# Performance work log

Hardware: AMD Instinct MI355X
Metric: run time of the kernel (lower is better)

The kernel has to match this reference:

```python
import jax, jax.numpy as jnp
import numpy as np

I_DIM = 512   # encoder feature size fed to CfC
UNITS = 1024  # AutoNCP total units (hidden_dim)
OUT = 128     # motor neurons (output_dim)
N = [538, 358, 128]                      # inter, command, motor layer sizes
IN_TOT = [I_DIM + N[0], N[0] + N[1], N[1] + N[2]]  # concat(input, h) width per layer
B, T = 512, 128


def setup_inputs() -> dict:
    key = jax.random.key(0)
    ks = jax.random.split(key, 40)
    d = {}
    d["x"] = jax.random.normal(ks[0], (B, T, I_DIM), jnp.float32)
    d["h0"] = jnp.zeros((B, UNITS), jnp.float32)
    ki = 1
    for l in range(3):
        it, n = IN_TOT[l], N[l]
        sp = (jax.random.uniform(ks[ki], (n, it - n)) < 0.5).astype(jnp.float32); ki += 1
        d[f"mask{l}"] = jnp.concatenate([sp, jnp.ones((n, n), jnp.float32)], axis=1)
        for name in ("Wff1", "Wff2", "Wta", "Wtb"):
            d[f"{name}_{l}"] = jax.random.normal(ks[ki], (n, it), jnp.float32) * float(1.0 / np.sqrt(it)); ki += 1
        for name in ("bff1", "bff2", "bta", "btb"):
            d[f"{name}_{l}"] = jnp.zeros((n,), jnp.float32)
    d["Wfc"] = jax.random.normal(ks[ki], (OUT, OUT), jnp.float32) * float(1.0 / np.sqrt(OUT))
    d["bfc"] = jnp.zeros((OUT,), jnp.float32)
    return d


def _cell(xin, h, p):
    # CfCCell, mode='default', no backbone, ts = 1.0
    W1, b1, W2, b2, Wa, ba, Wb, bb = p
    xc = jnp.concatenate([xin, h], axis=-1)           # (B, in+n)
    ff1 = jnp.tanh(xc @ W1.T + b1)
    ff2 = jnp.tanh(xc @ W2.T + b2)
    t_interp = jax.nn.sigmoid((xc @ Wa.T + ba) + (xc @ Wb.T + bb))
    return ff1 * (1.0 - t_interp) + t_interp * ff2


def reference(x, h0, mask0, Wff1_0, Wff2_0, Wta_0, Wtb_0, bff1_0, bff2_0, bta_0, btb_0,
              mask1, Wff1_1, Wff2_1, Wta_1, Wtb_1, bff1_1, bff2_1, bta_1, btb_1,
              mask2, Wff1_2, Wff2_2, Wta_2, Wtb_2, bff1_2, bff2_2, bta_2, btb_2,
              Wfc, bfc):
    params = (
        (Wff1_0 * mask0, bff1_0, Wff2_0 * mask0, bff2_0, Wta_0, bta_0, Wtb_0, btb_0),
        (Wff1_1 * mask1, bff1_1, Wff2_1 * mask1, bff2_1, Wta_1, bta_1, Wtb_1, btb_1),
        (Wff1_2 * mask2, bff1_2, Wff2_2 * mask2, bff2_2, Wta_2, bta_2, Wtb_2, btb_2),
    )
    hs0 = tuple(jnp.split(h0, [N[0], N[0] + N[1]], axis=1))

    def step(hs, x_t):
        inp = x_t
        new = []
        for l in range(3):
            inp = _cell(inp, hs[l], params[l])
            new.append(inp)
        return tuple(new), inp  # last layer (motor) is the cell output

    carry, outs = jax.lax.scan(step, hs0, jnp.swapaxes(x, 0, 1))
    outputs = jnp.swapaxes(outs, 0, 1)        # (B, T, OUT)
    hn = jnp.concatenate(carry, axis=1)       # (B, UNITS)
    predictions = outputs @ Wfc.T + bfc       # final nn.Linear
    return predictions, hn
```

## Files before the change

kernel.cpp:

```cpp
#include <hip/hip_runtime.h>
#include <stdint.h>

typedef __attribute__((ext_vector_type(8))) short short8;
typedef __attribute__((ext_vector_type(4))) float float4v;
typedef __attribute__((ext_vector_type(4))) unsigned short ushort4v;

constexpr int T = 128;
constexpr int NB = 512;
constexpr int NCH = 16;
constexpr int CBLK = 12;
constexpr int HS = 1056;

__device__ __forceinline__ float bf2f(ushort u) {
  union { float f; uint32_t i; } v; v.i = ((uint32_t)u) << 16; return v.f;
}
__device__ __forceinline__ ushort f2bf(float f) {
  union { float f; uint32_t i; } v; v.f = f;
  uint32_t i = v.i;
  uint32_t r = i + 0x7FFFu + ((i >> 16) & 1u);
  return (ushort)(r >> 16);
}

__device__ __forceinline__ unsigned long long coh_load8(const float* p) {
  return __hip_atomic_load(
      reinterpret_cast<unsigned long long*>(const_cast<float*>(p)),
      __ATOMIC_RELAXED, __HIP_MEMORY_SCOPE_SYSTEM);
}
__device__ __forceinline__ void coh_store8(float* p, float a, float b) {
  union { unsigned long long u; float f[2]; } v; v.f[0] = a; v.f[1] = b;
  __hip_atomic_store(reinterpret_cast<unsigned long long*>(p), v.u,
                     __ATOMIC_RELAXED, __HIP_MEMORY_SCOPE_SYSTEM);
}

__global__ __launch_bounds__(256) void pack_w(const float* __restrict__ W,
                                              const float* __restrict__ mask,
                                              ushort* __restrict__ out, int loOff,
                                              int NN, int IT, int NT, int KB,
                                              int POLD, int OLDLEN, int SOFF,
                                              int NEWLEN) {
  int idx = blockIdx.x * 256 + threadIdx.x;
  int total = KB * NT * 512;
  if (idx >= total) return;
  int jj   = idx & 7;
  int lane = (idx >> 3) & 63;
  int nt   = (idx >> 9) % NT;
  int kb   = (idx >> 9) / NT;
  int n = nt * 16 + (lane & 15);
  int p = kb * 32 + (lane >> 4) * 8 + jj;
  int src = -1;
  if (p < POLD) {
    if (p < OLDLEN) src = SOFF + p;
  } else {
    int q = p - POLD;
    if (q < NEWLEN) src = q;
  }
  float v = 0.f;
  if (n < NN && src >= 0) {
    v = W[(size_t)n * IT + src];
    if (mask) v *= mask[(size_t)n * IT + src];
  }
  ushort hi = f2bf(v);
  out[idx] = hi;
  out[loOff + idx] = f2bf(v - bf2f(hi));
}

template <int NTW, bool COH, int KB0, int KB1, int KOFF>
__device__ __forceinline__ void cell_range(
    ushort* __restrict__ Ah, ushort* __restrict__ Al,
    const float* __restrict__ aRow,
    const ushort* __restrict__ wfq, int nt0, int NT, int loOff,
    float4v (&acc)[2][NTW]) {
  constexpr int PD = 4;
  constexpr int LEN = KB1 - KB0;
  const int tid  = threadIdx.x;
  const int lane = tid & 63, quad = lane >> 4, l16 = lane & 15;
  const int sm = tid >> 3;
  const int sk = (tid & 7) * 4;

  short8 cbh[PD][NTW], cbl[PD][NTW];
  float4v av[PD];

  auto loadB = [&](int kb, short8* bh, short8* bl) {
#pragma unroll
    for (int w = 0; w < NTW; w++) {
      const size_t fo = ((size_t)(kb * NT + nt0 + w) * 64 + lane) * 8;
      bh[w] = *(const short8*)(wfq + fo);
      bl[w] = *(const short8*)(wfq + loOff + fo);
    }
  };
  auto loadA = [&](int kb) -> float4v {
    const float* p = aRow + (kb - KOFF) * 32 + sk;
    float4v r;
    if (COH) {
      union { unsigned long long u; float f[2]; } x0, x1;
      x0.u = coh_load8(p);
      x1.u = coh_load8(p + 2);
      r[0] = x0.f[0]; r[1] = x0.f[1]; r[2] = x1.f[0]; r[3] = x1.f[1];
    } else {
      r = *(const float4v*)p;
    }
    return r;
  };

#pragma unroll
  for (int i = 0; i < PD; i++) { av[i] = loadA(KB0 + i); loadB(KB0 + i, cbh[i], cbl[i]); }

  for (int kb0 = KB0; kb0 < KB1; kb0 += PD) {
#pragma unroll
    for (int u = 0; u < PD; u++) {
      const int kb = kb0 + u;
      if ((LEN % PD) && kb >= KB1) continue;
      const int ab = (kb & 1) * 1280;

      ushort4v hi4, lo4;
#pragma unroll
      for (int e = 0; e < 4; e++) {
        float v = av[u][e];
        ushort hi = f2bf(v);
        hi4[e] = hi;
        lo4[e] = f2bf(v - bf2f(hi));
      }
      *(ushort4v*)(Ah + ab + sm * 40 + sk) = hi4;
      *(ushort4v*)(Al + ab + sm * 40 + sk) = lo4;
      asm volatile("s_waitcnt lgkmcnt(0)\n\ts_barrier" ::: "memory");

#pragma unroll
      for (int mt = 0; mt < 2; mt++) {
        short8 ah = *(const short8*)&Ah[ab + (mt * 16 + l16) * 40 + quad * 8];
        short8 al = *(const short8*)&Al[ab + (mt * 16 + l16) * 40 + quad * 8];
#pragma unroll
        for (int w = 0; w < NTW; w++) {
          acc[mt][w] = __builtin_amdgcn_mfma_f32_16x16x32_bf16(ah, cbh[u][w], acc[mt][w], 0, 0, 0);
          acc[mt][w] = __builtin_amdgcn_mfma_f32_16x16x32_bf16(al, cbh[u][w], acc[mt][w], 0, 0, 0);
          acc[mt][w] = __builtin_amdgcn_mfma_f32_16x16x32_bf16(ah, cbl[u][w], acc[mt][w], 0, 0, 0);
        }
      }
      if (kb + PD < KB1) { av[u] = loadA(kb + PD); loadB(kb + PD, cbh[u], cbl[u]); }
    }
  }
}

template <int NTW>
__device__ __forceinline__ void cell_epilogue(
    float* __restrict__ Acc, float4v (&acc)[2][NTW],
    const float* const* __restrict__ bias4,
    int NN, int NNPAD, float* __restrict__ hout, float* __restrict__ out2,
    int b0, int n0) {
  const int tid = threadIdx.x;
  const int wave = tid >> 6, lane = tid & 63, quad = lane >> 4, l16 = lane & 15;
#pragma unroll
  for (int mt = 0; mt < 2; mt++)
#pragma unroll
    for (int w = 0; w < NTW; w++)
#pragma unroll
      for (int r = 0; r < 4; r++)
        Acc[(wave * 32 + mt * 16 + quad * 4 + r) * 50 + w * 16 + l16] = acc[mt][w][r];
  __syncthreads();
  constexpr int CW = 16 * NTW;
  for (int i4 = tid; i4 < 32 * (CW / 4); i4 += 256) {
    const int r = i4 / (CW / 4);
    const int c4 = (i4 % (CW / 4)) * 4;
    const int j0 = n0 + c4;
    if (j0 >= NNPAD) continue;
    float hv[4];
#pragma unroll
    for (int e = 0; e < 4; e++) {
      const int c = c4 + e, j = j0 + e;
      float h = 0.f;
      if (j < NN) {
        float v1 = Acc[(0 * 32 + r) * 50 + c] + bias4[0][j];
        float v2 = Acc[(1 * 32 + r) * 50 + c] + bias4[1][j];
        float va = Acc[(2 * 32 + r) * 50 + c] + bias4[2][j];
        float vb = Acc[(3 * 32 + r) * 50 + c] + bias4[3][j];
        float ff1 = tanhf(v1);
        float ff2 = tanhf(v2);
        float s = 1.f / (1.f + expf(-(va + vb)));
        h = ff1 * (1.f - s) + s * ff2;
      }
      hv[e] = h;
    }
    float* hp = hout + (size_t)(b0 + r) * HS + j0;
    coh_store8(hp, hv[0], hv[1]);
    coh_store8(hp + 2, hv[2], hv[3]);
    if (out2) {
      float4v o; o[0] = hv[0]; o[1] = hv[1]; o[2] = hv[2]; o[3] = hv[3];
      *(float4v*)(out2 + (size_t)(b0 + r) * 16384 + j0) = o;
    }
  }
}

struct PParams {
  const float* x;
  float* h0; float* h1;
  const ushort* wf0[4]; const ushort* wf1[4]; const ushort* wf2[4];
  int loOff0, loOff1, loOff2;
  const float* bias0[4]; const float* bias1[4]; const float* bias2[4];
  float* pred;
  int* bar;
};

__device__ __forceinline__ void bar_arrive(int* slot) {
  asm volatile("s_waitcnt vmcnt(0)" ::: "memory");
  __syncthreads();
  if (threadIdx.x == 0)
    __hip_atomic_fetch_add(slot, 1, __ATOMIC_RELAXED, __HIP_MEMORY_SCOPE_SYSTEM);
}
__device__ __forceinline__ void bar_wait(int* slot, int target) {
  if (threadIdx.x == 0) {
    while (__hip_atomic_load(slot, __ATOMIC_RELAXED, __HIP_MEMORY_SCOPE_SYSTEM) < target)
      __builtin_amdgcn_s_sleep(1);
  }
  __syncthreads();
}

__global__ __launch_bounds__(256, 1) void cfc_persistent(PParams p) {
  __shared__ ushort Ah[2 * 32 * 40];
  __shared__ ushort Al[2 * 32 * 40];
  __shared__ float  Acc[4 * 32 * 50];
  const int blk = blockIdx.x;
  const int c = blk / CBLK, ntp = blk % CBLK;
  const int b0 = c * 32;
  int* cbar = p.bar + c * (T * 3);
  const int wave = threadIdx.x >> 6;
  const int sm = threadIdx.x >> 3;
  const size_t rowoff = (size_t)(b0 + sm);

  for (int t = 0; t < T; t++) {
    float* hr = (t & 1) ? p.h1 : p.h0;
    float* hw = (t & 1) ? p.h0 : p.h1;
    const float* xRow  = p.x + rowoff * (T * 512) + (size_t)t * 512;
    const float* hrRow = hr + rowoff * HS;
    const float* hwRow = hw + rowoff * HS;

    float4v acc0[2][3];
#pragma unroll
    for (int i = 0; i < 2; i++)
#pragma unroll
      for (int w = 0; w < 3; w++) acc0[i][w] = float4v{0.f, 0.f, 0.f, 0.f};
    cell_range<3, false, 0, 16, 0 >(Ah, Al, xRow,  p.wf0[wave], ntp * 3, 36, p.loOff0, acc0);
    cell_range<3, true, 16, 33, 16>(Ah, Al, hrRow, p.wf0[wave], ntp * 3, 36, p.loOff0, acc0);
    cell_epilogue<3>(Acc, acc0, p.bias0, 538, 544, hw, nullptr, b0, ntp * 48);
    bar_arrive(cbar + t * 3);

    if (t && ntp >= 4) bar_wait(cbar + (t - 1) * 3 + 1, CBLK);
    float4v acc1[2][2];
#pragma unroll
    for (int i = 0; i < 2; i++)
#pragma unroll
      for (int w = 0; w < 2; w++) acc1[i][w] = float4v{0.f, 0.f, 0.f, 0.f};
    cell_range<2, true, 0, 12, 0 >(Ah, Al, hrRow + 544, p.wf1[wave], ntp * 2, 24, p.loOff1, acc1);
    bar_wait(cbar + t * 3, CBLK);
    cell_range<2, true, 12, 29, 12>(Ah, Al, hwRow, p.wf1[wave], ntp * 2, 24, p.loOff1, acc1);
    cell_epilogue<2>(Acc, acc1, p.bias1, 358, 384, hw + 544, nullptr, b0, ntp * 32);
    bar_arrive(cbar + t * 3 + 1);

    if (ntp < 4) {
      if (t) bar_wait(cbar + (t - 1) * 3 + 2, 4);
      float4v acc2[2][2];
#pragma unroll
      for (int i = 0; i < 2; i++)
#pragma unroll
        for (int w = 0; w < 2; w++) acc2[i][w] = float4v{0.f, 0.f, 0.f, 0.f};
      cell_range<2, true, 0, 4, 0>(Ah, Al, hrRow + 928, p.wf2[wave], ntp * 2, 8, p.loOff2, acc2);
      bar_wait(cbar + t * 3 + 1, CBLK);
      cell_range<2, true, 4, 16, 4>(Ah, Al, hwRow + 544, p.wf2[wave], ntp * 2, 8, p.loOff2, acc2);
      cell_epilogue<2>(Acc, acc2, p.bias2, 128, 128, hw + 928,
                       p.pred + (size_t)t * 128, b0, ntp * 32);
      bar_arrive(cbar + t * 3 + 2);
    }
  }
}

__global__ __launch_bounds__(256) void h_scatter(const float* __restrict__ src,
                                                 float* __restrict__ dst) {
  int idx = blockIdx.x * 256 + threadIdx.x;
  if (idx >= NB * HS) return;
  int b = idx / HS, u = idx % HS;
  int s = -1;
  if (u < 538) s = u;
  else if (u >= 544 && u < 902) s = 538 + (u - 544);
  else if (u >= 928) s = 896 + (u - 928);
  dst[idx] = (s >= 0) ? src[(size_t)b * 1024 + s] : 0.f;
}
__global__ __launch_bounds__(256) void h_gather(const float* __restrict__ src,
                                                float* __restrict__ dst) {
  int idx = blockIdx.x * 256 + threadIdx.x;
  if (idx >= NB * 1024) return;
  int b = idx / 1024, u = idx % 1024;
  int pu = (u < 538) ? u : (u < 896 ? (u - 538) + 544 : (u - 896) + 928);
  dst[idx] = src[(size_t)b * HS + pu];
}

__global__ __launch_bounds__(256)
void final_linear(float* __restrict__ io, const ushort* __restrict__ wfc_frag,
                  int loOff, const float* __restrict__ bfc) {
  __shared__ ushort Ah[64][136];
  __shared__ ushort Al[64][136];
  const int tid = threadIdx.x;
  const int wave = tid >> 6, lane = tid & 63, quad = lane >> 4, l16 = lane & 15;
  const size_t r0 = (size_t)blockIdx.x * 64;
  {
    const int row = tid >> 2;
    const int cb  = (tid & 3) * 32;
    const float* src = io + (r0 + row) * 128 + cb;
#pragma unroll
    for (int e = 0; e < 32; e++) {
      float v = src[e];
      ushort hi = f2bf(v);
      Ah[row][cb + e] = hi;
      Al[row][cb + e] = f2bf(v - bf2f(hi));
    }
  }
  __syncthreads();
  float4v acc[8];
#pragma unroll
  for (int i = 0; i < 8; i++) acc[i] = float4v{0.f, 0.f, 0.f, 0.f};
#pragma unroll
  for (int kb = 0; kb < 4; kb++) {
    short8 ah = *(const short8*)&Ah[wave * 16 + l16][kb * 32 + quad * 8];
    short8 al = *(const short8*)&Al[wave * 16 + l16][kb * 32 + quad * 8];
#pragma unroll
    for (int nt = 0; nt < 8; nt++) {
      const size_t fo = ((size_t)(kb * 8 + nt) * 64 + lane) * 8;
      short8 bh = *(const short8*)(wfc_frag + fo);
      short8 bl = *(const short8*)(wfc_frag + loOff + fo);
      acc[nt] = __builtin_amdgcn_mfma_f32_16x16x32_bf16(ah, bh, acc[nt], 0, 0, 0);
      acc[nt] = __builtin_amdgcn_mfma_f32_16x16x32_bf16(al, bh, acc[nt], 0, 0, 0);
      acc[nt] = __builtin_amdgcn_mfma_f32_16x16x32_bf16(ah, bl, acc[nt], 0, 0, 0);
    }
  }
  __syncthreads();
#pragma unroll
  for (int nt = 0; nt < 8; nt++) {
    int col = nt * 16 + l16;
    float bb = bfc[col];
#pragma unroll
    for (int r = 0; r < 4; r++) {
      int row = wave * 16 + quad * 4 + r;
      io[(r0 + row) * 128 + col] = acc[nt][r] + bb;
    }
  }
}

extern "C" void kernel_launch(void* const* d_in, const int* in_sizes, int n_in,
                              void* d_out, int out_size, void* d_ws, size_t ws_size,
                              hipStream_t stream) {
  const int maskIdx[3] = {2, 11, 20};
  const int wIdx[3]    = {3, 12, 21};
  const float* Wfc = (const float*)d_in[29];
  const float* bfc = (const float*)d_in[30];

  const int KBs[3]  = {33, 29, 16};
  const int NTs[3]  = {36, 24, 8};
  const int NNs[3]  = {538, 358, 128};
  const int ITs[3]  = {1050, 896, 486};
  const int POLDs[3]   = {0, 384, 128};
  const int OLDLENs[3] = {0, 358, 128};
  const int SOFFs[3]   = {0, 538, 358};
  const int NEWLENs[3] = {1050, 538, 358};

  ushort* ws = (ushort*)d_ws;
  size_t off = 0;
  ushort* wf[3][4];
  int loOff[3];
  for (int l = 0; l < 3; l++) {
    loOff[l] = KBs[l] * NTs[l] * 512;
    for (int q = 0; q < 4; q++) {
      wf[l][q] = ws + off;
      off += (size_t)2 * loOff[l];
    }
  }
  int wfcLo = 4 * 8 * 512;
  ushort* wfc_f = ws + off; off += (size_t)2 * wfcLo;
  float* hb0 = (float*)(ws + off); off += (size_t)NB * HS * 2;
  float* hb1 = (float*)(ws + off); off += (size_t)NB * HS * 2;
  int* bar = (int*)(ws + off); off += (size_t)NCH * T * 3 * 2;

  float* pred = (float*)d_out;
  float* hn   = (float*)d_out + (size_t)NB * T * 128;

  for (int l = 0; l < 3; l++) {
    int blocks = (loOff[l] + 255) / 256;
    for (int q = 0; q < 4; q++) {
      const float* m = (q < 2) ? (const float*)d_in[maskIdx[l]] : nullptr;
      pack_w<<<blocks, 256, 0, stream>>>((const float*)d_in[wIdx[l] + q], m, wf[l][q],
                                         loOff[l], NNs[l], ITs[l], NTs[l], KBs[l],
                                         POLDs[l], OLDLENs[l], SOFFs[l], NEWLENs[l]);
    }
  }
  pack_w<<<(wfcLo + 255) / 256, 256, 0, stream>>>(Wfc, nullptr, wfc_f, wfcLo,
                                                  128, 128, 8, 4, 0, 0, 0, 128);

  hipMemsetAsync(bar, 0, NCH * T * 3 * sizeof(int), stream);
  h_scatter<<<(NB * HS + 255) / 256, 256, 0, stream>>>((const float*)d_in[1], hb0);

  PParams p;
  p.x = (const float*)d_in[0];
  p.h0 = hb0; p.h1 = hb1;
  for (int q = 0; q < 4; q++) {
    p.wf0[q] = wf[0][q]; p.wf1[q] = wf[1][q]; p.wf2[q] = wf[2][q];
    p.bias0[q] = (const float*)d_in[7 + q];
    p.bias1[q] = (const float*)d_in[16 + q];
    p.bias2[q] = (const float*)d_in[25 + q];
  }
  p.loOff0 = loOff[0]; p.loOff1 = loOff[1]; p.loOff2 = loOff[2];
  p.pred = pred;
  p.bar = bar;

  cfc_persistent<<<NCH * CBLK, 256, 0, stream>>>(p);

  final_linear<<<(NB * T) / 64, 256, 0, stream>>>(pred, wfc_f, wfcLo, bfc);
  h_gather<<<(NB * 1024 + 255) / 256, 256, 0, stream>>>(hb0, hn);
}
```

Measured before the change: 5.867 ms.

## Halve per-step barriers, narrow atomic scope to agent, remap blocks across XCDs

The K-loop now stages two k-blocks into four LDS slots per barrier instead of one, which cuts workgroup barriers in the recurrent GEMM roughly in half. An odd trailing block is handled after the loop, and a sync is added before the epilogue. Coherent loads, stores and the inter-block barrier atomics drop from system scope to agent scope, which should make them cheaper. Block IDs are also remapped so the 12 blocks of each batch chunk are spread by XCD-interleaved index. The agent-scope change assumes every participant sits on one device, and the remap changes which blocks share an L2.

```diff
diff --git a/kernel.cpp b/kernel.cpp
--- a/kernel.cpp
+++ b/kernel.cpp
@@ -24,12 +24,12 @@
 __device__ __forceinline__ unsigned long long coh_load8(const float* p) {
   return __hip_atomic_load(
       reinterpret_cast<unsigned long long*>(const_cast<float*>(p)),
-      __ATOMIC_RELAXED, __HIP_MEMORY_SCOPE_SYSTEM);
+      __ATOMIC_RELAXED, __HIP_MEMORY_SCOPE_AGENT);
 }
 __device__ __forceinline__ void coh_store8(float* p, float a, float b) {
   union { unsigned long long u; float f[2]; } v; v.f[0] = a; v.f[1] = b;
   __hip_atomic_store(reinterpret_cast<unsigned long long*>(p), v.u,
-                     __ATOMIC_RELAXED, __HIP_MEMORY_SCOPE_SYSTEM);
+                     __ATOMIC_RELAXED, __HIP_MEMORY_SCOPE_AGENT);
 }
 
 __global__ __launch_bounds__(256) void pack_w(const float* __restrict__ W,
@@ -66,12 +66,14 @@
 
 template <int NTW, bool COH, int KB0, int KB1, int KOFF>
 __device__ __forceinline__ void cell_range(
-    ushort* __restrict__ Ah, ushort* __restrict__ Al,
+    ushort* __restrict__ Ast,
     const float* __restrict__ aRow,
     const ushort* __restrict__ wfq, int nt0, int NT, int loOff,
     float4v (&acc)[2][NTW]) {
   constexpr int PD = 4;
   constexpr int LEN = KB1 - KB0;
+  constexpr int LEN2 = LEN & ~1;
+  static_assert(LEN2 % PD == 0, "even part of every segment must be x4");
   const int tid  = threadIdx.x;
   const int lane = tid & 63, quad = lane >> 4, l16 = lane & 15;
   const int sm = tid >> 3;
@@ -80,7 +82,7 @@
   short8 cbh[PD][NTW], cbl[PD][NTW];
   float4v av[PD];
 
-  auto loadB = [&](int kb, short8* bh, short8* bl) {
+  auto loadB = [&](int kb, short8 (&bh)[NTW], short8 (&bl)[NTW]) {
 #pragma unroll
     for (int w = 0; w < NTW; w++) {
       const size_t fo = ((size_t)(kb * NT + nt0 + w) * 64 + lane) * 8;
@@ -101,42 +103,53 @@
     }
     return r;
   };
+  auto stageSlot = [&](int u, float4v a) {
+    ushort4v hi4, lo4;
+#pragma unroll
+    for (int e = 0; e < 4; e++) {
+      float v = a[e];
+      ushort hi = f2bf(v);
+      hi4[e] = hi;
+      lo4[e] = f2bf(v - bf2f(hi));
+    }
+    *(ushort4v*)(Ast + u * 2560 + sm * 40 + sk) = hi4;
+    *(ushort4v*)(Ast + u * 2560 + 1280 + sm * 40 + sk) = lo4;
+  };
+  auto mfmaSlot = [&](int u, const short8 (&bh)[NTW], const short8 (&bl)[NTW]) {
+#pragma unroll
+    for (int mt = 0; mt < 2; mt++) {
+      short8 ah = *(const short8*)(Ast + u * 2560 + (mt * 16 + l16) * 40 + quad * 8);
+      short8 al = *(const short8*)(Ast + u * 2560 + 1280 + (mt * 16 + l16) * 40 + quad * 8);
+#pragma unroll
+      for (int w = 0; w < NTW; w++) {
+        acc[mt][w] = __builtin_amdgcn_mfma_f32_16x16x32_bf16(ah, bh[w], acc[mt][w], 0, 0, 0);
+        acc[mt][w] = __builtin_amdgcn_mfma_f32_16x16x32_bf16(al, bh[w], acc[mt][w], 0, 0, 0);
+        acc[mt][w] = __builtin_amdgcn_mfma_f32_16x16x32_bf16(ah, bl[w], acc[mt][w], 0, 0, 0);
+      }
+    }
+  };
 
 #pragma unroll
   for (int i = 0; i < PD; i++) { av[i] = loadA(KB0 + i); loadB(KB0 + i, cbh[i], cbl[i]); }
 
-  for (int kb0 = KB0; kb0 < KB1; kb0 += PD) {
-#pragma unroll
-    for (int u = 0; u < PD; u++) {
-      const int kb = kb0 + u;
-      if ((LEN % PD) && kb >= KB1) continue;
-      const int ab = (kb & 1) * 1280;
-
-      ushort4v hi4, lo4;
-#pragma unroll
-      for (int e = 0; e < 4; e++) {
-        float v = av[u][e];
-        ushort hi = f2bf(v);
-        hi4[e] = hi;
-        lo4[e] = f2bf(v - bf2f(hi));
-      }
-      *(ushort4v*)(Ah + ab + sm * 40 + sk) = hi4;
-      *(ushort4v*)(Al + ab + sm * 40 + sk) = lo4;
+  for (int kb0 = KB0; kb0 < KB0 + LEN2; kb0 += PD) {
+#pragma unroll
+    for (int up = 0; up < 2; up++) {
+      const int u0 = up * 2, u1 = up * 2 + 1;
+      const int kb = kb0 + up * 2;
+      stageSlot(u0, av[u0]);
+      stageSlot(u1, av[u1]);
       asm volatile("s_waitcnt lgkmcnt(0)\n\ts_barrier" ::: "memory");
-
-#pragma unroll
-      for (int mt = 0; mt < 2; mt++) {
-        short8 ah = *(const short8*)&Ah[ab + (mt * 16 + l16) * 40 + quad * 8];
-        short8 al = *(const short8*)&Al[ab + (mt * 16 + l16) * 40 + quad * 8];
-#pragma unroll
-        for (int w = 0; w < NTW; w++) {
-          acc[mt][w] = __builtin_amdgcn_mfma_f32_16x16x32_bf16(ah, cbh[u][w], acc[mt][w], 0, 0, 0);
-          acc[mt][w] = __builtin_amdgcn_mfma_f32_16x16x32_bf16(al, cbh[u][w], acc[mt][w], 0, 0, 0);
-          acc[mt][w] = __builtin_amdgcn_mfma_f32_16x16x32_bf16(ah, cbl[u][w], acc[mt][w], 0, 0, 0);
-        }
-      }
-      if (kb + PD < KB1) { av[u] = loadA(kb + PD); loadB(kb + PD, cbh[u], cbl[u]); }
-    }
+      mfmaSlot(u0, cbh[u0], cbl[u0]);
+      mfmaSlot(u1, cbh[u1], cbl[u1]);
+      if (kb + PD < KB1)     { av[u0] = loadA(kb + PD);     loadB(kb + PD,     cbh[u0], cbl[u0]); }
+      if (kb + 1 + PD < KB1) { av[u1] = loadA(kb + 1 + PD); loadB(kb + 1 + PD, cbh[u1], cbl[u1]); }
+    }
+  }
+  if (LEN & 1) {
+    stageSlot(0, av[0]);
+    asm volatile("s_waitcnt lgkmcnt(0)\n\ts_barrier" ::: "memory");
+    mfmaSlot(0, cbh[0], cbl[0]);
   }
 }
 
@@ -148,6 +161,7 @@
     int b0, int n0) {
   const int tid = threadIdx.x;
   const int wave = tid >> 6, lane = tid & 63, quad = lane >> 4, l16 = lane & 15;
+  __syncthreads();
 #pragma unroll
   for (int mt = 0; mt < 2; mt++)
 #pragma unroll
@@ -203,22 +217,23 @@
   asm volatile("s_waitcnt vmcnt(0)" ::: "memory");
   __syncthreads();
   if (threadIdx.x == 0)
-    __hip_atomic_fetch_add(slot, 1, __ATOMIC_RELAXED, __HIP_MEMORY_SCOPE_SYSTEM);
+    __hip_atomic_fetch_add(slot, 1, __ATOMIC_RELAXED, __HIP_MEMORY_SCOPE_AGENT);
 }
 __device__ __forceinline__ void bar_wait(int* slot, int target) {
   if (threadIdx.x == 0) {
-    while (__hip_atomic_load(slot, __ATOMIC_RELAXED, __HIP_MEMORY_SCOPE_SYSTEM) < target)
+    while (__hip_atomic_load(slot, __ATOMIC_RELAXED, __HIP_MEMORY_SCOPE_AGENT) < target)
       __builtin_amdgcn_s_sleep(1);
   }
   __syncthreads();
 }
 
 __global__ __launch_bounds__(256, 1) void cfc_persistent(PParams p) {
-  __shared__ ushort Ah[2 * 32 * 40];
-  __shared__ ushort Al[2 * 32 * 40];
+  __shared__ ushort Ast[4 * 2560];
   __shared__ float  Acc[4 * 32 * 50];
-  const int blk = blockIdx.x;
-  const int c = blk / CBLK, ntp = blk % CBLK;
+  const int phys = blockIdx.x;
+  const int s = (phys & 7) * 24 + (phys >> 3);
+  const int ntp = s >> 4;
+  const int c   = s & 15;
   const int b0 = c * 32;
   int* cbar = p.bar + c * (T * 3);
   const int wave = threadIdx.x >> 6;
@@ -237,8 +252,8 @@
     for (int i = 0; i < 2; i++)
 #pragma unroll
       for (int w = 0; w < 3; w++) acc0[i][w] = float4v{0.f, 0.f, 0.f, 0.f};
-    cell_range<3, false, 0, 16, 0 >(Ah, Al, xRow,  p.wf0[wave], ntp * 3, 36, p.loOff0, acc0);
-    cell_range<3, true, 16, 33, 16>(Ah, Al, hrRow, p.wf0[wave], ntp * 3, 36, p.loOff0, acc0);
+    cell_range<3, false, 0, 16, 0 >(Ast, xRow,  p.wf0[wave], ntp * 3, 36, p.loOff0, acc0);
+    cell_range<3, true, 16, 33, 16>(Ast, hrRow, p.wf0[wave], ntp * 3, 36, p.loOff0, acc0);
     cell_epilogue<3>(Acc, acc0, p.bias0, 538, 544, hw, nullptr, b0, ntp * 48);
     bar_arrive(cbar + t * 3);
 
@@ -248,9 +263,9 @@
     for (int i = 0; i < 2; i++)
 #pragma unroll
       for (int w = 0; w < 2; w++) acc1[i][w] = float4v{0.f, 0.f, 0.f, 0.f};
-    cell_range<2, true, 0, 12, 0 >(Ah, Al, hrRow + 544, p.wf1[wave], ntp * 2, 24, p.loOff1, acc1);
+    cell_range<2, true, 0, 12, 0 >(Ast, hrRow + 544, p.wf1[wave], ntp * 2, 24, p.loOff1, acc1);
     bar_wait(cbar + t * 3, CBLK);
-    cell_range<2, true, 12, 29, 12>(Ah, Al, hwRow, p.wf1[wave], ntp * 2, 24, p.loOff1, acc1);
+    cell_range<2, true, 12, 29, 12>(Ast, hwRow, p.wf1[wave], ntp * 2, 24, p.loOff1, acc1);
     cell_epilogue<2>(Acc, acc1, p.bias1, 358, 384, hw + 544, nullptr, b0, ntp * 32);
     bar_arrive(cbar + t * 3 + 1);
 
@@ -261,9 +276,9 @@
       for (int i = 0; i < 2; i++)
 #pragma unroll
         for (int w = 0; w < 2; w++) acc2[i][w] = float4v{0.f, 0.f, 0.f, 0.f};
-      cell_range<2, true, 0, 4, 0>(Ah, Al, hrRow + 928, p.wf2[wave], ntp * 2, 8, p.loOff2, acc2);
+      cell_range<2, true, 0, 4, 0>(Ast, hrRow + 928, p.wf2[wave], ntp * 2, 8, p.loOff2, acc2);
       bar_wait(cbar + t * 3 + 1, CBLK);
-      cell_range<2, true, 4, 16, 4>(Ah, Al, hwRow + 544, p.wf2[wave], ntp * 2, 8, p.loOff2, acc2);
+      cell_range<2, true, 4, 16, 4>(Ast, hwRow + 544, p.wf2[wave], ntp * 2, 8, p.loOff2, acc2);
       cell_epilogue<2>(Acc, acc2, p.bias2, 128, 128, hw + 928,
                        p.pred + (size_t)t * 128, b0, ntp * 32);
       bar_arrive(cbar + t * 3 + 2);
```

Result: faster. 5.749 ms (-2.0%).

## Store hidden state as split bf16 and stage whole A panels in LDS

Applied to the files above, without the earlier changes.

The hidden state is now kept in global memory as pre-split bf16 hi/lo pairs, written once in the epilogue, instead of fp32 values that every consumer had to split again. Each cell stage now copies the whole A operand (x or h segment) into a large LDS buffer up front. This replaces the per-k-block convert, LDS write and barrier loop with barrier-free double-buffered LDS reads inside the MFMA loop. Atomics and barriers are narrowed from system to agent scope, and blocks are remapped across chunks. In exchange there is more LDS, extra staging barriers, and an extra rounding step when h is stored as hi+lo.

```diff
diff --git a/kernel.cpp b/kernel.cpp
--- a/kernel.cpp
+++ b/kernel.cpp
@@ -21,15 +21,14 @@
   return (ushort)(r >> 16);
 }
 
-__device__ __forceinline__ unsigned long long coh_load8(const float* p) {
+__device__ __forceinline__ unsigned long long coh_load8u(const ushort* p) {
   return __hip_atomic_load(
-      reinterpret_cast<unsigned long long*>(const_cast<float*>(p)),
-      __ATOMIC_RELAXED, __HIP_MEMORY_SCOPE_SYSTEM);
-}
-__device__ __forceinline__ void coh_store8(float* p, float a, float b) {
-  union { unsigned long long u; float f[2]; } v; v.f[0] = a; v.f[1] = b;
-  __hip_atomic_store(reinterpret_cast<unsigned long long*>(p), v.u,
-                     __ATOMIC_RELAXED, __HIP_MEMORY_SCOPE_SYSTEM);
+      reinterpret_cast<unsigned long long*>(const_cast<ushort*>(p)),
+      __ATOMIC_RELAXED, __HIP_MEMORY_SCOPE_AGENT);
+}
+__device__ __forceinline__ void coh_store8u(ushort* p, unsigned long long v) {
+  __hip_atomic_store(reinterpret_cast<unsigned long long*>(p), v,
+                     __ATOMIC_RELAXED, __HIP_MEMORY_SCOPE_AGENT);
 }
 
 __global__ __launch_bounds__(256) void pack_w(const float* __restrict__ W,
@@ -64,78 +63,102 @@
   out[loOff + idx] = f2bf(v - bf2f(hi));
 }
 
-template <int NTW, bool COH, int KB0, int KB1, int KOFF>
-__device__ __forceinline__ void cell_range(
-    ushort* __restrict__ Ah, ushort* __restrict__ Al,
-    const float* __restrict__ aRow,
-    const ushort* __restrict__ wfq, int nt0, int NT, int loOff,
-    float4v (&acc)[2][NTW]) {
-  constexpr int PD = 4;
-  constexpr int LEN = KB1 - KB0;
-  const int tid  = threadIdx.x;
-  const int lane = tid & 63, quad = lane >> 4, l16 = lane & 15;
-  const int sm = tid >> 3;
-  const int sk = (tid & 7) * 4;
+template <int SEGC, int S>
+__device__ __forceinline__ void stage_h(ushort* __restrict__ Abuf,
+                                        const ushort* __restrict__ hiG,
+                                        const ushort* __restrict__ loG) {
+  constexpr int CH = SEGC / 32;
+  const int r  = threadIdx.x >> 3;
+  const int c0 = (threadIdx.x & 7) * (SEGC / 8);
+  const ushort* hg = hiG + (size_t)r * HS + c0;
+  const ushort* lg = loG + (size_t)r * HS + c0;
+  unsigned long long vh[CH], vl[CH];
+#pragma unroll
+  for (int i = 0; i < CH; i++) vh[i] = coh_load8u(hg + i * 4);
+#pragma unroll
+  for (int i = 0; i < CH; i++) vl[i] = coh_load8u(lg + i * 4);
+  ushort* hd = Abuf + r * S + c0;
+  ushort* ld = Abuf + 32 * S + r * S + c0;
+#pragma unroll
+  for (int i = 0; i < CH; i++) *(unsigned long long*)(hd + i * 4) = vh[i];
+#pragma unroll
+  for (int i = 0; i < CH; i++) *(unsigned long long*)(ld + i * 4) = vl[i];
+}
+
+template <int S>
+__device__ __forceinline__ void stage_x(ushort* __restrict__ Abuf,
+                                        const float* __restrict__ xG) {
+  const int r = threadIdx.x >> 3;
+  const int q = threadIdx.x & 7;
+  const float* src = xG + (size_t)r * (T * 512);
+  ushort* hd = Abuf + r * S;
+  ushort* ld = Abuf + 32 * S + r * S;
+#pragma unroll
+  for (int i = 0; i < 8; i++) {
+    const int c = q * 8 + i * 64;
+    float4v a = *(const float4v*)(src + c);
+    float4v b = *(const float4v*)(src + c + 4);
+    ushort4v ha, la, hb, lb;
+#pragma unroll
+    for (int e = 0; e < 4; e++) {
+      ushort h1 = f2bf(a[e]); ha[e] = h1; la[e] = f2bf(a[e] - bf2f(h1));
+      ushort h2 = f2bf(b[e]); hb[e] = h2; lb[e] = f2bf(b[e] - bf2f(h2));
+    }
+    *(ushort4v*)(hd + c) = ha; *(ushort4v*)(hd + c + 4) = hb;
+    *(ushort4v*)(ld + c) = la; *(ushort4v*)(ld + c + 4) = lb;
+  }
+}
+
+template <int NTW, int PD, int KB0, int KB1, int KOFF, int S>
+__device__ __forceinline__ void krange(const ushort* __restrict__ Abuf,
+                                       const ushort* __restrict__ wfq, int nt0,
+                                       int NT, int loOff, float4v (&acc)[2][NTW]) {
+  static_assert((PD & 1) == 0 && (KB0 & 1) == 0, "static parity needs even");
+  const int lane = threadIdx.x & 63, quad = lane >> 4, l16 = lane & 15;
+  const int ab = l16 * S + quad * 8 - KOFF * 32;
 
   short8 cbh[PD][NTW], cbl[PD][NTW];
-  float4v av[PD];
-
-  auto loadB = [&](int kb, short8* bh, short8* bl) {
+  short8 ah[2][2], al[2][2];
+
+  auto loadB = [&](int kb, int u) {
 #pragma unroll
     for (int w = 0; w < NTW; w++) {
       const size_t fo = ((size_t)(kb * NT + nt0 + w) * 64 + lane) * 8;
-      bh[w] = *(const short8*)(wfq + fo);
-      bl[w] = *(const short8*)(wfq + loOff + fo);
+      cbh[u][w] = *(const short8*)(wfq + fo);
+      cbl[u][w] = *(const short8*)(wfq + loOff + fo);
     }
   };
-  auto loadA = [&](int kb) -> float4v {
-    const float* p = aRow + (kb - KOFF) * 32 + sk;
-    float4v r;
-    if (COH) {
-      union { unsigned long long u; float f[2]; } x0, x1;
-      x0.u = coh_load8(p);
-      x1.u = coh_load8(p + 2);
-      r[0] = x0.f[0]; r[1] = x0.f[1]; r[2] = x1.f[0]; r[3] = x1.f[1];
-    } else {
-      r = *(const float4v*)p;
-    }
-    return r;
+  auto dsA = [&](int kb, int par) {
+    const int o = ab + kb * 32;
+    ah[par][0] = *(const short8*)(Abuf + o);
+    ah[par][1] = *(const short8*)(Abuf + o + 16 * S);
+    al[par][0] = *(const short8*)(Abuf + o + 32 * S);
+    al[par][1] = *(const short8*)(Abuf + o + 48 * S);
   };
 
 #pragma unroll
-  for (int i = 0; i < PD; i++) { av[i] = loadA(KB0 + i); loadB(KB0 + i, cbh[i], cbl[i]); }
+  for (int i = 0; i < PD; i++)
+    if (KB0 + i < KB1) loadB(KB0 + i, i);
+  dsA(KB0, 0);
 
   for (int kb0 = KB0; kb0 < KB1; kb0 += PD) {
 #pragma unroll
     for (int u = 0; u < PD; u++) {
       const int kb = kb0 + u;
-      if ((LEN % PD) && kb >= KB1) continue;
-      const int ab = (kb & 1) * 1280;
-
-      ushort4v hi4, lo4;
-#pragma unroll
-      for (int e = 0; e < 4; e++) {
-        float v = av[u][e];
-        ushort hi = f2bf(v);
-        hi4[e] = hi;
-        lo4[e] = f2bf(v - bf2f(hi));
+      if (kb < KB1) {
+        const int par = (KB0 + u) & 1;
+        if (kb + 1 < KB1) dsA(kb + 1, par ^ 1);
+#pragma unroll
+        for (int mt = 0; mt < 2; mt++) {
+#pragma unroll
+          for (int w = 0; w < NTW; w++) {
+            acc[mt][w] = __builtin_amdgcn_mfma_f32_16x16x32_bf16(ah[par][mt], cbh[u][w], acc[mt][w], 0, 0, 0);
+            acc[mt][w] = __builtin_amdgcn_mfma_f32_16x16x32_bf16(al[par][mt], cbh[u][w], acc[mt][w], 0, 0, 0);
+            acc[mt][w] = __builtin_amdgcn_mfma_f32_16x16x32_bf16(ah[par][mt], cbl[u][w], acc[mt][w], 0, 0, 0);
+          }
+        }
+        if (kb + PD < KB1) loadB(kb + PD, u);
       }
-      *(ushort4v*)(Ah + ab + sm * 40 + sk) = hi4;
-      *(ushort4v*)(Al + ab + sm * 40 + sk) = lo4;
-      asm volatile("s_waitcnt lgkmcnt(0)\n\ts_barrier" ::: "memory");
-
-#pragma unroll
-      for (int mt = 0; mt < 2; mt++) {
-        short8 ah = *(const short8*)&Ah[ab + (mt * 16 + l16) * 40 + quad * 8];
-        short8 al = *(const short8*)&Al[ab + (mt * 16 + l16) * 40 + quad * 8];
-#pragma unroll
-        for (int w = 0; w < NTW; w++) {
-          acc[mt][w] = __builtin_amdgcn_mfma_f32_16x16x32_bf16(ah, cbh[u][w], acc[mt][w], 0, 0, 0);
-          acc[mt][w] = __builtin_amdgcn_mfma_f32_16x16x32_bf16(al, cbh[u][w], acc[mt][w], 0, 0, 0);
-          acc[mt][w] = __builtin_amdgcn_mfma_f32_16x16x32_bf16(ah, cbl[u][w], acc[mt][w], 0, 0, 0);
-        }
-      }
-      if (kb + PD < KB1) { av[u] = loadA(kb + PD); loadB(kb + PD, cbh[u], cbl[u]); }
     }
   }
 }
@@ -144,10 +167,11 @@
 __device__ __forceinline__ void cell_epilogue(
     float* __restrict__ Acc, float4v (&acc)[2][NTW],
     const float* const* __restrict__ bias4,
-    int NN, int NNPAD, float* __restrict__ hout, float* __restrict__ out2,
-    int b0, int n0) {
+    int NN, int NNPAD, ushort* __restrict__ hiOut, ushort* __restrict__ loOut,
+    float* __restrict__ out2, int b0, int n0) {
   const int tid = threadIdx.x;
   const int wave = tid >> 6, lane = tid & 63, quad = lane >> 4, l16 = lane & 15;
+  __syncthreads();
 #pragma unroll
   for (int mt = 0; mt < 2; mt++)
 #pragma unroll
@@ -162,6 +186,7 @@
     const int c4 = (i4 % (CW / 4)) * 4;
     const int j0 = n0 + c4;
     if (j0 >= NNPAD) continue;
+    union { ushort u[4]; unsigned long long ll; } ph, pl;
     float hv[4];
 #pragma unroll
     for (int e = 0; e < 4; e++) {
@@ -178,10 +203,13 @@
         h = ff1 * (1.f - s) + s * ff2;
       }
       hv[e] = h;
-    }
-    float* hp = hout + (size_t)(b0 + r) * HS + j0;
-    coh_store8(hp, hv[0], hv[1]);
-    coh_store8(hp + 2, hv[2], hv[3]);
+      ushort hh = f2bf(h);
+      ph.u[e] = hh;
+      pl.u[e] = f2bf(h - bf2f(hh));
+    }
+    const size_t ro = (size_t)(b0 + r) * HS + j0;
+    coh_store8u(hiOut + ro, ph.ll);
+    coh_store8u(loOut + ro, pl.ll);
     if (out2) {
       float4v o; o[0] = hv[0]; o[1] = hv[1]; o[2] = hv[2]; o[3] = hv[3];
       *(float4v*)(out2 + (size_t)(b0 + r) * 16384 + j0) = o;
@@ -191,7 +219,7 @@
 
 struct PParams {
   const float* x;
-  float* h0; float* h1;
+  ushort* h0hi; ushort* h0lo; ushort* h1hi; ushort* h1lo;
   const ushort* wf0[4]; const ushort* wf1[4]; const ushort* wf2[4];
   int loOff0, loOff1, loOff2;
   const float* bias0[4]; const float* bias1[4]; const float* bias2[4];
@@ -203,68 +231,85 @@
   asm volatile("s_waitcnt vmcnt(0)" ::: "memory");
   __syncthreads();
   if (threadIdx.x == 0)
-    __hip_atomic_fetch_add(slot, 1, __ATOMIC_RELAXED, __HIP_MEMORY_SCOPE_SYSTEM);
+    __hip_atomic_fetch_add(slot, 1, __ATOMIC_RELAXED, __HIP_MEMORY_SCOPE_AGENT);
 }
 __device__ __forceinline__ void bar_wait(int* slot, int target) {
   if (threadIdx.x == 0) {
-    while (__hip_atomic_load(slot, __ATOMIC_RELAXED, __HIP_MEMORY_SCOPE_SYSTEM) < target)
+    while (__hip_atomic_load(slot, __ATOMIC_RELAXED, __HIP_MEMORY_SCOPE_AGENT) < target)
       __builtin_amdgcn_s_sleep(1);
   }
   __syncthreads();
 }
 
 __global__ __launch_bounds__(256, 1) void cfc_persistent(PParams p) {
-  __shared__ ushort Ah[2 * 32 * 40];
-  __shared__ ushort Al[2 * 32 * 40];
+  __shared__ ushort Abuf[2 * 32 * 552];
   __shared__ float  Acc[4 * 32 * 50];
-  const int blk = blockIdx.x;
-  const int c = blk / CBLK, ntp = blk % CBLK;
+  const int phys = blockIdx.x;
+  const int s = (phys & 7) * 24 + (phys >> 3);
+  const int ntp = s >> 4;
+  const int c   = s & 15;
   const int b0 = c * 32;
   int* cbar = p.bar + c * (T * 3);
   const int wave = threadIdx.x >> 6;
-  const int sm = threadIdx.x >> 3;
-  const size_t rowoff = (size_t)(b0 + sm);
+  const ushort* wq0 = p.wf0[wave];
+  const ushort* wq1 = p.wf1[wave];
+  const ushort* wq2 = p.wf2[wave];
+  const size_t bo = (size_t)b0 * HS;
 
   for (int t = 0; t < T; t++) {
-    float* hr = (t & 1) ? p.h1 : p.h0;
-    float* hw = (t & 1) ? p.h0 : p.h1;
-    const float* xRow  = p.x + rowoff * (T * 512) + (size_t)t * 512;
-    const float* hrRow = hr + rowoff * HS;
-    const float* hwRow = hw + rowoff * HS;
-
+    const bool odd = t & 1;
+    const ushort* rdHi = odd ? p.h1hi : p.h0hi;
+    const ushort* rdLo = odd ? p.h1lo : p.h0lo;
+    ushort* wrHi = odd ? p.h0hi : p.h1hi;
+    ushort* wrLo = odd ? p.h0lo : p.h1lo;
+
+    stage_x<520>(Abuf, p.x + (size_t)b0 * (T * 512) + (size_t)t * 512);
+    __syncthreads();
     float4v acc0[2][3];
 #pragma unroll
     for (int i = 0; i < 2; i++)
 #pragma unroll
       for (int w = 0; w < 3; w++) acc0[i][w] = float4v{0.f, 0.f, 0.f, 0.f};
-    cell_range<3, false, 0, 16, 0 >(Ah, Al, xRow,  p.wf0[wave], ntp * 3, 36, p.loOff0, acc0);
-    cell_range<3, true, 16, 33, 16>(Ah, Al, hrRow, p.wf0[wave], ntp * 3, 36, p.loOff0, acc0);
-    cell_epilogue<3>(Acc, acc0, p.bias0, 538, 544, hw, nullptr, b0, ntp * 48);
+    krange<3, 4, 0, 16, 0, 520>(Abuf, wq0, ntp * 3, 36, p.loOff0, acc0);
+    __syncthreads();
+    stage_h<544, 552>(Abuf, rdHi + bo, rdLo + bo);
+    __syncthreads();
+    krange<3, 4, 16, 33, 16, 552>(Abuf, wq0, ntp * 3, 36, p.loOff0, acc0);
+    cell_epilogue<3>(Acc, acc0, p.bias0, 538, 544, wrHi, wrLo, nullptr, b0, ntp * 48);
     bar_arrive(cbar + t * 3);
 
     if (t && ntp >= 4) bar_wait(cbar + (t - 1) * 3 + 1, CBLK);
+    stage_h<384, 392>(Abuf, rdHi + bo + 544, rdLo + bo + 544);
+    __syncthreads();
     float4v acc1[2][2];
 #pragma unroll
     for (int i = 0; i < 2; i++)
 #pragma unroll
       for (int w = 0; w < 2; w++) acc1[i][w] = float4v{0.f, 0.f, 0.f, 0.f};
-    cell_range<2, true, 0, 12, 0 >(Ah, Al, hrRow + 544, p.wf1[wave], ntp * 2, 24, p.loOff1, acc1);
+    krange<2, 4, 0, 12, 0, 392>(Abuf, wq1, ntp * 2, 24, p.loOff1, acc1);
     bar_wait(cbar + t * 3, CBLK);
-    cell_range<2, true, 12, 29, 12>(Ah, Al, hwRow, p.wf1[wave], ntp * 2, 24, p.loOff1, acc1);
-    cell_epilogue<2>(Acc, acc1, p.bias1, 358, 384, hw + 544, nullptr, b0, ntp * 32);
+    stage_h<544, 552>(Abuf, wrHi + bo, wrLo + bo);
+    __syncthreads();
+    krange<2, 4, 12, 29, 12, 552>(Abuf, wq1, ntp * 2, 24, p.loOff1, acc1);
+    cell_epilogue<2>(Acc, acc1, p.bias1, 358, 384, wrHi + 544, wrLo + 544,
+                     nullptr, b0, ntp * 32);
     bar_arrive(cbar + t * 3 + 1);
 
     if (ntp < 4) {
       if (t) bar_wait(cbar + (t - 1) * 3 + 2, 4);
+      stage_h<128, 136>(Abuf, rdHi + bo + 928, rdLo + bo + 928);
+      __syncthreads();
       float4v acc2[2][2];
 #pragma unroll
       for (int i = 0; i < 2; i++)
 #pragma unroll
         for (int w = 0; w < 2; w++) acc2[i][w] = float4v{0.f, 0.f, 0.f, 0.f};
-      cell_range<2, true, 0, 4, 0>(Ah, Al, hrRow + 928, p.wf2[wave], ntp * 2, 8, p.loOff2, acc2);
+      krange<2, 4, 0, 4, 0, 136>(Abuf, wq2, ntp * 2, 8, p.loOff2, acc2);
       bar_wait(cbar + t * 3 + 1, CBLK);
-      cell_range<2, true, 4, 16, 4>(Ah, Al, hwRow + 544, p.wf2[wave], ntp * 2, 8, p.loOff2, acc2);
-      cell_epilogue<2>(Acc, acc2, p.bias2, 128, 128, hw + 928,
+      stage_h<384, 392>(Abuf, wrHi + bo + 544, wrLo + bo + 544);
+      __syncthreads();
+      krange<2, 4, 4, 16, 4, 392>(Abuf, wq2, ntp * 2, 8, p.loOff2, acc2);
+      cell_epilogue<2>(Acc, acc2, p.bias2, 128, 128, wrHi + 928, wrLo + 928,
                        p.pred + (size_t)t * 128, b0, ntp * 32);
       bar_arrive(cbar + t * 3 + 2);
     }
@@ -272,7 +317,8 @@
 }
 
 __global__ __launch_bounds__(256) void h_scatter(const float* __restrict__ src,
-                                                 float* __restrict__ dst) {
+                                                 ushort* __restrict__ hi,
+                                                 ushort* __restrict__ lo) {
   int idx = blockIdx.x * 256 + threadIdx.x;
   if (idx >= NB * HS) return;
   int b = idx / HS, u = idx % HS;
@@ -280,15 +326,20 @@
   if (u < 538) s = u;
   else if (u >= 544 && u < 902) s = 538 + (u - 544);
   else if (u >= 928) s = 896 + (u - 928);
-  dst[idx] = (s >= 0) ? src[(size_t)b * 1024 + s] : 0.f;
-}
-__global__ __launch_bounds__(256) void h_gather(const float* __restrict__ src,
+  float v = (s >= 0) ? src[(size_t)b * 1024 + s] : 0.f;
+  ushort h = f2bf(v);
+  hi[idx] = h;
+  lo[idx] = f2bf(v - bf2f(h));
+}
+__global__ __launch_bounds__(256) void h_gather(const ushort* __restrict__ hi,
+                                                const ushort* __restrict__ lo,
                                                 float* __restrict__ dst) {
   int idx = blockIdx.x * 256 + threadIdx.x;
   if (idx >= NB * 1024) return;
   int b = idx / 1024, u = idx % 1024;
   int pu = (u < 538) ? u : (u < 896 ? (u - 538) + 544 : (u - 896) + 928);
-  dst[idx] = src[(size_t)b * HS + pu];
+  size_t o = (size_t)b * HS + pu;
+  dst[idx] = bf2f(hi[o]) + bf2f(lo[o]);
 }
 
 __global__ __launch_bounds__(256)
@@ -372,8 +423,10 @@
   }
   int wfcLo = 4 * 8 * 512;
   ushort* wfc_f = ws + off; off += (size_t)2 * wfcLo;
-  float* hb0 = (float*)(ws + off); off += (size_t)NB * HS * 2;
-  float* hb1 = (float*)(ws + off); off += (size_t)NB * HS * 2;
+  ushort* h0hi = ws + off; off += (size_t)NB * HS;
+  ushort* h0lo = ws + off; off += (size_t)NB * HS;
+  ushort* h1hi = ws + off; off += (size_t)NB * HS;
+  ushort* h1lo = ws + off; off += (size_t)NB * HS;
   int* bar = (int*)(ws + off); off += (size_t)NCH * T * 3 * 2;
 
   float* pred = (float*)d_out;
@@ -392,11 +445,12 @@
                                                   128, 128, 8, 4, 0, 0, 0, 128);
 
   hipMemsetAsync(bar, 0, NCH * T * 3 * sizeof(int), stream);
-  h_scatter<<<(NB * HS + 255) / 256, 256, 0, stream>>>((const float*)d_in[1], hb0);
+  h_scatter<<<(NB * HS + 255) / 256, 256, 0, stream>>>((const float*)d_in[1],
+                                                       h0hi, h0lo);
 
   PParams p;
   p.x = (const float*)d_in[0];
-  p.h0 = hb0; p.h1 = hb1;
+  p.h0hi = h0hi; p.h0lo = h0lo; p.h1hi = h1hi; p.h1lo = h1lo;
   for (int q = 0; q < 4; q++) {
     p.wf0[q] = wf[0][q]; p.wf1[q] = wf[1][q]; p.wf2[q] = wf[2][q];
     p.bias0[q] = (const float*)d_in[7 + q];
@@ -410,5 +464,5 @@
   cfc_persistent<<<NCH * CBLK, 256, 0, stream>>>(p);
 
   final_linear<<<(NB * T) / 64, 256, 0, stream>>>(pred, wfc_f, wfcLo, bfc);
-  h_gather<<<(NB * 1024 + 255) / 256, 256, 0, stream>>>(hb0, hn);
-}
+  h_gather<<<(NB * 1024 + 255) / 256, 256, 0, stream>>>(h0hi, h0lo, hn);
+}
```

New measurement: 13.20 ms. 2.25x slower.
